# Kernel tuning notes

Hardware: AMD Instinct MI355X
Metric: run time of the kernel (lower is better)

The kernel has to match this reference:

```python
import jax, jax.numpy as jnp
import numpy as np

NUM_EMBEDDINGS = 8192
EMBEDDING_DIM = 256
COMMITMENT_COST = 0.25
DECAY = 0.99
EPS = 1e-05


def setup_inputs() -> dict:
    key = jax.random.key(0)
    k1, k2, k3 = jax.random.split(key, 3)
    z = jax.random.normal(k1, (32, 1024, EMBEDDING_DIM), dtype=jnp.float32)
    embedding = jax.random.normal(k2, (NUM_EMBEDDINGS, EMBEDDING_DIM), dtype=jnp.float32)
    ema_cluster_size = jnp.zeros((NUM_EMBEDDINGS,), dtype=jnp.float32)
    ema_w = jax.random.normal(k3, (NUM_EMBEDDINGS, EMBEDDING_DIM), dtype=jnp.float32)
    return {"z": z, "embedding": embedding,
            "ema_cluster_size": ema_cluster_size, "ema_w": ema_w}


def reference(z, embedding, ema_cluster_size, ema_w):
    K, D = embedding.shape
    flat_z = z.reshape(-1, D)                                     # [N, D]

    # squared-distance matrix [N, K]: |z|^2 + |e|^2 - 2 z.e
    distances = (jnp.sum(flat_z * flat_z, axis=1, keepdims=True)
                 + jnp.sum(embedding * embedding, axis=1)
                 - 2.0 * flat_z @ embedding.T)
    indices = jnp.argmin(distances, axis=1)                       # [N] int

    # one-hot @ embedding == row gather
    z_q_flat = embedding[indices]                                 # [N, D]

    # --- training-mode EMA update (one-hot sums == scatter-adds) ---
    counts = jax.ops.segment_sum(jnp.ones_like(indices, dtype=flat_z.dtype),
                                 indices, num_segments=K)         # sum(encodings, 0)
    new_cluster_size = ema_cluster_size * DECAY + (1.0 - DECAY) * counts
    dw = jax.ops.segment_sum(flat_z, indices, num_segments=K)     # encodings.T @ flat_z
    new_ema_w = ema_w * DECAY + (1.0 - DECAY) * dw
    n = jnp.sum(new_cluster_size)
    cluster_size = (new_cluster_size + EPS) / (n + K * EPS) * n
    new_embedding = new_ema_w / cluster_size[:, None]

    # commitment loss uses z_q computed with the OLD embedding (detached)
    loss = COMMITMENT_COST * jnp.mean(
        (jax.lax.stop_gradient(z_q_flat) - flat_z) ** 2)
    # straight-through estimator
    z_q = flat_z + jax.lax.stop_gradient(z_q_flat - flat_z)
    z_q = z_q.reshape(z.shape)
    return z_q, loss, indices, new_embedding, new_cluster_size, new_ema_w
```

## Files before the change

kernel.cpp:

```cpp
#include <hip/hip_runtime.h>
#include <cfloat>

#define K_CODES 8192
#define DIM     256
#define NROWS   32768

#define O_ZQ    0
#define O_LOSS  8388608
#define O_IDX   8388609
#define O_NEMB  8421377
#define O_NCS   10518529
#define O_NEMAW 10526721

#define NCH          2
#define CODES_PER_CH (K_CODES / NCH)
#define NT_TILES     (CODES_PER_CH / 256)

typedef __attribute__((ext_vector_type(8))) short short8;
typedef __attribute__((ext_vector_type(4))) float floatx4;

__device__ __forceinline__ unsigned short f2bf_rne(float x) {
    unsigned u = __float_as_uint(x);
    u += 0x7fffu + ((u >> 16) & 1u);
    return (unsigned short)(u >> 16);
}
__device__ __forceinline__ float bf2f(unsigned short h) {
    return __uint_as_float(((unsigned)h) << 16);
}
__device__ __forceinline__ void async16(const void* g, void* l) {
    __builtin_amdgcn_global_load_lds(
        (const __attribute__((address_space(1))) void*)g,
        (__attribute__((address_space(3))) void*)l, 16, 0, 0);
}

__global__ void k_prep(const float* __restrict__ z, const float* __restrict__ emb,
                       unsigned short* __restrict__ zcat, unsigned short* __restrict__ ecat,
                       float* __restrict__ esq, int* __restrict__ zero16k) {
    const int b = blockIdx.x;
    if (b < 8192) {
        const int i = b * 256 + threadIdx.x;
        const int row = i >> 6;
        const int col = (i & 63) << 2;
        float4 v = ((const float4*)z)[i];
        float nx = -2.0f * v.x, ny = -2.0f * v.y, nz = -2.0f * v.z, nw = -2.0f * v.w;
        ushort4 h, l;
        h.x = f2bf_rne(nx); l.x = f2bf_rne(nx - bf2f(h.x));
        h.y = f2bf_rne(ny); l.y = f2bf_rne(ny - bf2f(h.y));
        h.z = f2bf_rne(nz); l.z = f2bf_rne(nz - bf2f(h.z));
        h.w = f2bf_rne(nw); l.w = f2bf_rne(nw - bf2f(h.w));
        *(ushort4*)&zcat[(size_t)row * 512 + col]       = h;
        *(ushort4*)&zcat[(size_t)row * 512 + 256 + col] = l;
    } else {
        const int gid  = (b - 8192) * 256 + threadIdx.x;
        if (gid < 2 * K_CODES) zero16k[gid] = 0;
        const int code = gid >> 6;
        const int lane = gid & 63;
        const int col  = lane << 2;
        float4 v = ((const float4*)emb)[code * 64 + lane];
        ushort4 h, l;
        h.x = f2bf_rne(v.x); l.x = f2bf_rne(v.x - bf2f(h.x));
        h.y = f2bf_rne(v.y); l.y = f2bf_rne(v.y - bf2f(h.y));
        h.z = f2bf_rne(v.z); l.z = f2bf_rne(v.z - bf2f(h.z));
        h.w = f2bf_rne(v.w); l.w = f2bf_rne(v.w - bf2f(h.w));
        *(ushort4*)&ecat[(size_t)code * 512 + col]       = h;
        *(ushort4*)&ecat[(size_t)code * 512 + 256 + col] = l;
        float s = fmaf(v.x, v.x, fmaf(v.y, v.y, fmaf(v.z, v.z, v.w * v.w)));
#pragma unroll
        for (int off = 32; off > 0; off >>= 1) s += __shfl_down(s, off, 64);
        if (lane == 0) esq[code] = s;
    }
}

#define STAGE(AS, BS, BGP, offa, offb)                                          \
    do {                                                                        \
        _Pragma("unroll")                                                       \
        for (int c_ = 0; c_ < 6; ++c_) {                                        \
            const int u_ = w * 6 + c_;                                          \
            if (u_ < 8)                                                         \
                async16(aGlob + (size_t)u_ * 8192 + (offa), &AS[u_ * 512]);     \
            else                                                                \
                async16((BGP) + (size_t)(u_ - 8) * 8192 + (offb),               \
                        &BS[(u_ - 8) * 512]);                                   \
        }                                                                       \
    } while (0)

#define COMPUTE(AS, BS)                                                         \
    do {                                                                        \
        short8 bf_[8];                                                          \
        _Pragma("unroll")                                                       \
        for (int j_ = 0; j_ < 8; ++j_)                                          \
            bf_[j_] = *(const short8*)&BS[(wcol + j_ * 16 + m) * 32 + xo];      \
        _Pragma("unroll")                                                       \
        for (int i_ = 0; i_ < 4; ++i_) {                                        \
            const short8 af_ =                                                  \
                *(const short8*)&AS[(wrow + i_ * 16 + m) * 32 + xo];            \
            _Pragma("unroll")                                                   \
            for (int j_ = 0; j_ < 8; ++j_)                                      \
                acc[i_][j_] = __builtin_amdgcn_mfma_f32_16x16x32_bf16(          \
                    af_, bf_[j_], acc[i_][j_], 0, 0, 0);                        \
        }                                                                       \
    } while (0)

__global__ __launch_bounds__(256, 2) void k_argmin_mfma(
        const unsigned short* __restrict__ zcat, const unsigned short* __restrict__ ecat,
        const float* __restrict__ esq,
        float* __restrict__ part_v, int* __restrict__ part_i) {
    __shared__ __align__(16) unsigned short a0_s[128 * 32];
    __shared__ __align__(16) unsigned short a1_s[128 * 32];
    __shared__ __align__(16) unsigned short b0_s[256 * 32];
    __shared__ __align__(16) unsigned short b1_s[256 * 32];
    const int t    = threadIdx.x;
    const int w    = t >> 6;
    const int lane = t & 63;
    const int quad = lane >> 4;
    const int m    = lane & 15;
    const int wrow = (w >> 1) * 64;
    const int wcol = (w & 1) * 128;
    const int row0   = blockIdx.x * 128;
    const int cbase0 = blockIdx.y * CODES_PER_CH;

    const int    swz    = (((lane & 3) ^ ((lane >> 3) & 3)) << 3);
    const size_t srcrow = (size_t)(lane >> 2) * 512 + swz;
    const unsigned short* aGlob = zcat + (size_t)row0 * 512 + srcrow;
    const unsigned short* bGlob = ecat + (size_t)cbase0 * 512 + srcrow;

    const int xo = ((quad ^ ((m >> 1) & 3)) << 3);

    float    best_v[16];
    unsigned best_p[4];
#pragma unroll
    for (int r = 0; r < 16; ++r) best_v[r] = FLT_MAX;
#pragma unroll
    for (int i = 0; i < 4; ++i) best_p[i] = 0u;

    STAGE(a0_s, b0_s, bGlob, 0, 0);
    __syncthreads();

    for (int nt = 0; nt < NT_TILES; ++nt) {
        const int cb = cbase0 + nt * 256;
        const unsigned short* bNT  = bGlob + (size_t)nt * 131072;
        const unsigned short* bNT1 = bNT + 131072;
        floatx4 acc[4][8];
#pragma unroll
        for (int j = 0; j < 8; ++j) {
            const float es = esq[cb + wcol + j * 16 + m];
#pragma unroll
            for (int i = 0; i < 4; ++i) acc[i][j] = (floatx4){es, es, es, es};
        }

#pragma unroll 1
        for (int kk2 = 0; kk2 < 12; ++kk2) {
            {
                const int nk0 = kk2 * 64 + 32;
                STAGE(a1_s, b1_s, bNT, (nk0 & 255) | ((nk0 & 512) >> 1), nk0 & 511);
                COMPUTE(a0_s, b0_s);
                __syncthreads();
            }
            {
                if (kk2 < 11) {
                    const int nk0 = kk2 * 64 + 64;
                    STAGE(a0_s, b0_s, bNT, (nk0 & 255) | ((nk0 & 512) >> 1), nk0 & 511);
                } else if (nt + 1 < NT_TILES) {
                    STAGE(a0_s, b0_s, bNT1, 0, 0);
                }
                COMPUTE(a1_s, b1_s);
                __syncthreads();
            }
        }
#pragma unroll
        for (int j = 0; j < 8; ++j) {
            const unsigned cand = (unsigned)(nt * 8 + j);
#pragma unroll
            for (int i = 0; i < 4; ++i)
#pragma unroll
                for (int reg = 0; reg < 4; ++reg) {
                    const float s = acc[i][j][reg];
                    const int r = i * 4 + reg;
                    if (s < best_v[r]) {
                        best_v[r] = s;
                        best_p[i] = (best_p[i] & ~(255u << (reg * 8))) | (cand << (reg * 8));
                    }
                }
        }
    }
    __syncthreads();
    float* redv = (float*)a0_s;
    int*   redi = (int*)b0_s;
#pragma unroll
    for (int i = 0; i < 4; ++i)
#pragma unroll
        for (int reg = 0; reg < 4; ++reg) {
            const int r = i * 4 + reg;
            const unsigned b = (best_p[i] >> (reg * 8)) & 255u;
            float v  = best_v[r];
            int   bi = cbase0 + (int)(b >> 3) * 256 + wcol + (int)(b & 7) * 16 + m;
#pragma unroll
            for (int off = 1; off < 16; off <<= 1) {
                const float ov = __shfl_xor(v, off, 64);
                const int   oi = __shfl_xor(bi, off, 64);
                if (ov < v || (ov == v && oi < bi)) { v = ov; bi = oi; }
            }
            if (m == 0) {
                const int row = wrow + i * 16 + quad * 4 + reg;
                redv[row * 2 + (w & 1)] = v;
                redi[row * 2 + (w & 1)] = bi;
            }
        }
    __syncthreads();
    if (t < 128) {
        const float v0 = redv[t * 2], v1 = redv[t * 2 + 1];
        const int   i0 = redi[t * 2], i1 = redi[t * 2 + 1];
        const bool  b1 = (v1 < v0) || (v1 == v0 && i1 < i0);
        const size_t o = (size_t)blockIdx.y * NROWS + blockIdx.x * 128 + t;
        part_v[o] = b1 ? v1 : v0;
        part_i[o] = b1 ? i1 : i0;
    }
}

#undef STAGE
#undef COMPUTE

__global__ void k_reduce_part(const float* __restrict__ pv, const int* __restrict__ pi,
                              int* __restrict__ idx_i, float* __restrict__ idx_f,
                              int* __restrict__ counts) {
    const int r = blockIdx.x * blockDim.x + threadIdx.x;
    float v = pv[r]; int bi = pi[r];
#pragma unroll
    for (int c = 1; c < NCH; ++c) {
        const float v2 = pv[(size_t)c * NROWS + r];
        const int   i2 = pi[(size_t)c * NROWS + r];
        if (v2 < v || (v2 == v && i2 < bi)) { v = v2; bi = i2; }
    }
    idx_i[r] = bi;
    idx_f[r] = (float)bi;
    atomicAdd(&counts[bi], 1);
}

__global__ void k_scan_ncs(const int* __restrict__ counts, const float* __restrict__ ema_cs,
                           int* __restrict__ offsets, float* __restrict__ ncs_out,
                           float* __restrict__ ntot) {
    __shared__ int   wsum[16];
    __shared__ float red[16];
    const int t = threadIdx.x;
    const int lane = t & 63, w = t >> 6;
    int c[8]; int s = 0; float fs = 0.0f;
#pragma unroll
    for (int u = 0; u < 8; ++u) {
        c[u] = counts[t * 8 + u]; s += c[u];
        const float v = fmaf(0.99f, ema_cs[t * 8 + u], 0.01f * (float)c[u]);
        ncs_out[t * 8 + u] = v;
        fs += v;
    }
    int inc = s;
#pragma unroll
    for (int off = 1; off < 64; off <<= 1) {
        const int n = __shfl_up(inc, off, 64);
        if (lane >= off) inc += n;
    }
#pragma unroll
    for (int off = 32; off > 0; off >>= 1) fs += __shfl_down(fs, off, 64);
    if (lane == 63) wsum[w] = inc;
    if (lane == 0)  red[w]  = fs;
    __syncthreads();
    if (t < 16) {
        int v = wsum[t];
#pragma unroll
        for (int off = 1; off < 16; off <<= 1) {
            const int n = __shfl_up(v, off, 64);
            if (t >= off) v += n;
        }
        wsum[t] = v;
        float fv = red[t];
#pragma unroll
        for (int off = 8; off > 0; off >>= 1) fv += __shfl_down(fv, off, 16);
        if (t == 0) *ntot = fv;
    }
    __syncthreads();
    int base = (w > 0 ? wsum[w - 1] : 0) + (inc - s);
#pragma unroll
    for (int u = 0; u < 8; ++u) { offsets[t * 8 + u] = base; base += c[u]; }
}

__global__ void k_zq(const float* __restrict__ z, const float* __restrict__ emb,
                     const int* __restrict__ idx_i, const int* __restrict__ offsets,
                     int* __restrict__ cursor, int* __restrict__ buckets,
                     float* __restrict__ zq, float* __restrict__ losspart) {
    __shared__ float lred[4];
    const int t = threadIdx.x;
    const int wr = t >> 6, lane = t & 63;
    const int row = blockIdx.x * 4 + wr;
    const int code = idx_i[row];
    float4 zv = ((const float4*)z)[row * 64 + lane];
    float4 ev = ((const float4*)emb)[(size_t)code * 64 + lane];
    float4 o = make_float4(zv.x + (ev.x - zv.x), zv.y + (ev.y - zv.y),
                           zv.z + (ev.z - zv.z), zv.w + (ev.w - zv.w));
    ((float4*)zq)[row * 64 + lane] = o;
    float dx = ev.x - zv.x, dy = ev.y - zv.y, dz = ev.z - zv.z, dw = ev.w - zv.w;
    float s = fmaf(dx, dx, fmaf(dy, dy, fmaf(dz, dz, dw * dw)));
#pragma unroll
    for (int off = 32; off > 0; off >>= 1) s += __shfl_down(s, off, 64);
    if (lane == 0) {
        lred[wr] = s;
        const int pos = atomicAdd(&cursor[code], 1);
        buckets[offsets[code] + pos] = row;
    }
    __syncthreads();
    if (t == 0) losspart[blockIdx.x] = (lred[0] + lred[1]) + (lred[2] + lred[3]);
}

__global__ void k_dw_nemb(const float* __restrict__ z, const float* __restrict__ ema_w,
                          const int* __restrict__ counts, const int* __restrict__ offsets,
                          const int* __restrict__ buckets, const float* __restrict__ ncs,
                          const float* __restrict__ ntot_p, const float* __restrict__ losspart,
                          float* __restrict__ nemaw, float* __restrict__ nemb,
                          float* __restrict__ loss_out) {
    __shared__ float lred[4];
    if (blockIdx.x == K_CODES) {
        const int t = threadIdx.x;
        float s = 0.0f;
        for (int i = t; i < 8192; i += 256) s += losspart[i];
#pragma unroll
        for (int off = 32; off > 0; off >>= 1) s += __shfl_down(s, off, 64);
        if ((t & 63) == 0) lred[t >> 6] = s;
        __syncthreads();
        if (t == 0)
            *loss_out = 0.25f * ((lred[0] + lred[1]) + (lred[2] + lred[3])) / 8388608.0f;
        return;
    }
    const int code = blockIdx.x;
    const int d    = threadIdx.x;
    const int cnt  = counts[code];
    const int off  = offsets[code];
    float acc = 0.0f;
    for (int it = 0; it < cnt; ++it)
        acc += z[(size_t)buckets[off + it] * DIM + d];
    const float wv = fmaf(0.99f, ema_w[(size_t)code * DIM + d], 0.01f * acc);
    nemaw[(size_t)code * DIM + d] = wv;
    const float n  = *ntot_p;
    const float cs = (ncs[code] + 1e-5f) * (n / (n + (float)K_CODES * 1e-5f));
    nemb[(size_t)code * DIM + d] = wv / cs;
}

#define BM   64
#define BN   128
#define LSTR 36

__global__ void k_esq_zero_fb(const float* __restrict__ emb, float* __restrict__ esq,
                              float* __restrict__ zbuf) {
    const int gid  = blockIdx.x * blockDim.x + threadIdx.x;
    if (gid < K_CODES + 2) zbuf[gid] = 0.0f;
    const int code = gid >> 6;
    const int lane = gid & 63;
    float4 v = ((const float4*)emb)[code * 64 + lane];
    float s = fmaf(v.x, v.x, fmaf(v.y, v.y, fmaf(v.z, v.z, v.w * v.w)));
#pragma unroll
    for (int off = 32; off > 0; off >>= 1) s += __shfl_down(s, off, 64);
    if (lane == 0) esq[code] = s;
}

__global__ void k_init_nemaw_fb(const float* __restrict__ ema_w, float* __restrict__ out) {
    const int i = blockIdx.x * blockDim.x + threadIdx.x;
    float4 v = ((const float4*)ema_w)[i];
    ((float4*)out)[i] = make_float4(0.99f * v.x, 0.99f * v.y, 0.99f * v.z, 0.99f * v.w);
}

__global__ __launch_bounds__(256, 2) void k_argmin_fb(
        const float* __restrict__ z, const float* __restrict__ emb,
        const float* __restrict__ esq, int* __restrict__ idx_i, float* __restrict__ idx_f) {
    __shared__ float z_s[BM * LSTR];
    __shared__ float e_s[BN * LSTR];
    const int t = threadIdx.x, tx = t & 15, ty = t >> 4;
    const int row0 = blockIdx.x * BM;
    float best[4]; int bidx[4];
#pragma unroll
    for (int r = 0; r < 4; ++r) { best[r] = FLT_MAX; bidx[r] = 0; }
    for (int k0 = 0; k0 < K_CODES; k0 += BN) {
        float acc[4][8];
#pragma unroll
        for (int r = 0; r < 4; ++r)
#pragma unroll
            for (int c = 0; c < 8; ++c) acc[r][c] = 0.0f;
        for (int d0 = 0; d0 < DIM; d0 += 32) {
            __syncthreads();
#pragma unroll
            for (int i = 0; i < 2; ++i) {
                int f = i * 256 + t, r = f >> 3, c4 = (f & 7) << 2;
                *(float4*)&z_s[r * LSTR + c4] =
                    *(const float4*)(z + (size_t)(row0 + r) * DIM + d0 + c4);
            }
#pragma unroll
            for (int i = 0; i < 4; ++i) {
                int f = i * 256 + t, c = f >> 3, c4 = (f & 7) << 2;
                *(float4*)&e_s[c * LSTR + c4] =
                    *(const float4*)(emb + (size_t)(k0 + c) * DIM + d0 + c4);
            }
            __syncthreads();
#pragma unroll
            for (int dd = 0; dd < 32; dd += 4) {
                float4 a[4], b[8];
#pragma unroll
                for (int j = 0; j < 4; ++j)
                    a[j] = *(const float4*)&z_s[(ty * 4 + j) * LSTR + dd];
#pragma unroll
                for (int j = 0; j < 8; ++j)
                    b[j] = *(const float4*)&e_s[(tx + 16 * j) * LSTR + dd];
#pragma unroll
                for (int r = 0; r < 4; ++r)
#pragma unroll
                    for (int c = 0; c < 8; ++c) {
                        acc[r][c] = fmaf(a[r].x, b[c].x, acc[r][c]);
                        acc[r][c] = fmaf(a[r].y, b[c].y, acc[r][c]);
                        acc[r][c] = fmaf(a[r].z, b[c].z, acc[r][c]);
                        acc[r][c] = fmaf(a[r].w, b[c].w, acc[r][c]);
                    }
            }
        }
#pragma unroll
        for (int c = 0; c < 8; ++c) {
            const int code = k0 + tx + 16 * c;
            const float es = esq[code];
#pragma unroll
            for (int r = 0; r < 4; ++r) {
                float s = fmaf(-2.0f, acc[r][c], es);
                if (s < best[r] || (s == best[r] && code < bidx[r])) {
                    best[r] = s; bidx[r] = code;
                }
            }
        }
    }
    __syncthreads();
    float* rv = e_s; int* ri = (int*)z_s;
#pragma unroll
    for (int r = 0; r < 4; ++r) {
        rv[(ty * 4 + r) * 16 + tx] = best[r];
        ri[(ty * 4 + r) * 16 + tx] = bidx[r];
    }
    __syncthreads();
    if (t < 64) {
        float mv = rv[t * 16]; int mi = ri[t * 16];
#pragma unroll
        for (int i = 1; i < 16; ++i) {
            float v = rv[t * 16 + i]; int vi = ri[t * 16 + i];
            if (v < mv || (v == mv && vi < mi)) { mv = v; mi = vi; }
        }
        idx_i[row0 + t] = mi;
        idx_f[row0 + t] = (float)mi;
    }
}

__global__ void k_gather_fb(const float* __restrict__ z, const float* __restrict__ emb,
                            const int* __restrict__ idx_i, float* __restrict__ zq,
                            float* __restrict__ nemaw, float* __restrict__ counts,
                            float* __restrict__ loss) {
    const int gid  = blockIdx.x * blockDim.x + threadIdx.x;
    const int row  = gid >> 6;
    const int lane = gid & 63;
    const int code = idx_i[row];
    float4 zv = ((const float4*)z)[row * 64 + lane];
    float4 ev = ((const float4*)emb)[(size_t)code * 64 + lane];
    float4 o = make_float4(zv.x + (ev.x - zv.x), zv.y + (ev.y - zv.y),
                           zv.z + (ev.z - zv.z), zv.w + (ev.w - zv.w));
    ((float4*)zq)[row * 64 + lane] = o;
    float dx = ev.x - zv.x, dy = ev.y - zv.y, dz = ev.z - zv.z, dw = ev.w - zv.w;
    float s = fmaf(dx, dx, fmaf(dy, dy, fmaf(dz, dz, dw * dw)));
#pragma unroll
    for (int off = 32; off > 0; off >>= 1) s += __shfl_down(s, off, 64);
    if (lane == 0) { atomicAdd(loss, s); atomicAdd(&counts[code], 1.0f); }
    float* base = nemaw + (size_t)code * DIM + lane * 4;
    atomicAdd(base + 0, 0.01f * zv.x);
    atomicAdd(base + 1, 0.01f * zv.y);
    atomicAdd(base + 2, 0.01f * zv.z);
    atomicAdd(base + 3, 0.01f * zv.w);
}

__global__ void k_ncs_fb(const float* __restrict__ ema_cs, const float* __restrict__ counts,
                         float* __restrict__ ncs_out, float* __restrict__ ntot,
                         const float* __restrict__ loss_in, float* __restrict__ loss_out) {
    __shared__ float red[16];
    const int t = threadIdx.x;
    float s = 0.0f;
    for (int i = t; i < K_CODES; i += 1024) {
        float v = fmaf(0.99f, ema_cs[i], 0.01f * counts[i]);
        ncs_out[i] = v; s += v;
    }
#pragma unroll
    for (int off = 32; off > 0; off >>= 1) s += __shfl_down(s, off, 64);
    if ((t & 63) == 0) red[t >> 6] = s;
    __syncthreads();
    if (t < 16) {
        float v = red[t];
#pragma unroll
        for (int off = 8; off > 0; off >>= 1) v += __shfl_down(v, off, 16);
        if (t == 0) { *ntot = v; *loss_out = 0.25f * (*loss_in) / 8388608.0f; }
    }
}

__global__ void k_nemb_fb(const float* __restrict__ nemaw, const float* __restrict__ ncs,
                          const float* __restrict__ ntot_p, float* __restrict__ nemb) {
    const int i4 = blockIdx.x * blockDim.x + threadIdx.x;
    const int k  = i4 >> 6;
    const float n   = *ntot_p;
    const float inv = n / (n + (float)K_CODES * 1e-5f);
    const float cs  = (ncs[k] + 1e-5f) * inv;
    float4 wv = ((const float4*)nemaw)[i4];
    ((float4*)nemb)[i4] = make_float4(wv.x / cs, wv.y / cs, wv.z / cs, wv.w / cs);
}

extern "C" void kernel_launch(void* const* d_in, const int* in_sizes, int n_in,
                              void* d_out, int out_size, void* d_ws, size_t ws_size,
                              hipStream_t stream) {
    const float* z      = (const float*)d_in[0];
    const float* emb    = (const float*)d_in[1];
    const float* ema_cs = (const float*)d_in[2];
    const float* ema_w  = (const float*)d_in[3];
    float* out = (float*)d_out;
    char* wsb = (char*)d_ws;

    unsigned short* zcat    = (unsigned short*)wsb;
    unsigned short* ecat    = (unsigned short*)(wsb + 33554432);
    float*          part_v  = (float*)(wsb + 41943040);
    int*            part_i  = (int*)  (wsb + 42467328);
    float*          esq     = (float*)(wsb + 42991616);
    int*            ws_idx  = (int*)  (wsb + 43024384);
    int*            counts  = (int*)  (wsb + 43155456);
    int*            cursor  = (int*)  (wsb + 43188224);
    int*            offsets = (int*)  (wsb + 43220992);
    int*            buckets = (int*)  (wsb + 43253760);
    float*          lpart   = (float*)(wsb + 43384832);
    float*          ws_loss = (float*)(wsb + 43417600);
    float*          ws_ntot = ws_loss + 1;

    if (ws_size >= (size_t)43417616) {
        k_prep       <<<10240, 256, 0, stream>>>(z, emb, zcat, ecat, esq, counts);
        k_argmin_mfma<<<dim3(NROWS / 128, NCH), 256, 0, stream>>>(
            zcat, ecat, esq, part_v, part_i);
        k_reduce_part<<<NROWS / 256, 256, 0, stream>>>(part_v, part_i, ws_idx,
                                                       out + O_IDX, counts);
        k_scan_ncs   <<<1, 1024, 0, stream>>>(counts, ema_cs, offsets,
                                              out + O_NCS, ws_ntot);
        k_zq         <<<NROWS / 4, 256, 0, stream>>>(z, emb, ws_idx, offsets, cursor,
                                                     buckets, out + O_ZQ, lpart);
        k_dw_nemb    <<<K_CODES + 1, 256, 0, stream>>>(z, ema_w, counts, offsets, buckets,
                                                       out + O_NCS, ws_ntot, lpart,
                                                       out + O_NEMAW, out + O_NEMB,
                                                       out + O_LOSS);
    } else {
        int*   f_idx    = (int*)wsb;
        float* f_counts = (float*)(wsb + 131072);
        float* f_loss   = f_counts + K_CODES;
        float* f_ntot   = f_loss + 1;
        float* f_esq    = (float*)(wsb + 163856);
        k_esq_zero_fb  <<<2048, 256, 0, stream>>>(emb, f_esq, f_counts);
        k_init_nemaw_fb<<<2048, 256, 0, stream>>>(ema_w, out + O_NEMAW);
        k_argmin_fb    <<<NROWS / BM, 256, 0, stream>>>(z, emb, f_esq, f_idx, out + O_IDX);
        k_gather_fb    <<<NROWS / 4, 256, 0, stream>>>(z, emb, f_idx, out + O_ZQ,
                                                       out + O_NEMAW, f_counts, f_loss);
        k_ncs_fb       <<<1, 1024, 0, stream>>>(ema_cs, f_counts, out + O_NCS, f_ntot,
                                                f_loss, out + O_LOSS);
        k_nemb_fb      <<<2048, 256, 0, stream>>>(out + O_NEMAW, out + O_NCS, f_ntot,
                                                  out + O_NEMB);
    }
}
```

Before: 670.5 us.

## Triple-buffer LDS staging in argmin MFMA kernel with one barrier per step

```diff
diff --git a/kernel.cpp b/kernel.cpp
--- a/kernel.cpp
+++ b/kernel.cpp
@@ -15,6 +15,9 @@
 #define NCH          2
 #define CODES_PER_CH (K_CODES / NCH)
 #define NT_TILES     (CODES_PER_CH / 256)
+#define BUF_U        12288
+#define STEPS_NT     24
+#define LDS_BYTES    (3 * BUF_U * 2)
 
 typedef __attribute__((ext_vector_type(8))) short short8;
 typedef __attribute__((ext_vector_type(4))) float floatx4;
@@ -71,29 +74,31 @@
     }
 }
 
-#define STAGE(AS, BS, BGP, offa, offb)                                          \
+#define STAGE3(obufU, BGP, offa, offb)                                          \
     do {                                                                        \
         _Pragma("unroll")                                                       \
         for (int c_ = 0; c_ < 6; ++c_) {                                        \
             const int u_ = w * 6 + c_;                                          \
             if (u_ < 8)                                                         \
-                async16(aGlob + (size_t)u_ * 8192 + (offa), &AS[u_ * 512]);     \
+                async16(aGlob + (size_t)u_ * 8192 + (offa),                     \
+                        &s_all[(obufU) + u_ * 512]);                            \
             else                                                                \
                 async16((BGP) + (size_t)(u_ - 8) * 8192 + (offb),               \
-                        &BS[(u_ - 8) * 512]);                                   \
+                        &s_all[(obufU) + 4096 + (u_ - 8) * 512]);               \
         }                                                                       \
     } while (0)
 
-#define COMPUTE(AS, BS)                                                         \
+#define COMPUTE3(obufU)                                                         \
     do {                                                                        \
         short8 bf_[8];                                                          \
         _Pragma("unroll")                                                       \
         for (int j_ = 0; j_ < 8; ++j_)                                          \
-            bf_[j_] = *(const short8*)&BS[(wcol + j_ * 16 + m) * 32 + xo];      \
+            bf_[j_] = *(const short8*)                                          \
+                &s_all[(obufU) + 4096 + (wcol + j_ * 16 + m) * 32 + xo];        \
         _Pragma("unroll")                                                       \
         for (int i_ = 0; i_ < 4; ++i_) {                                        \
-            const short8 af_ =                                                  \
-                *(const short8*)&AS[(wrow + i_ * 16 + m) * 32 + xo];            \
+            const short8 af_ = *(const short8*)                                 \
+                &s_all[(obufU) + (wrow + i_ * 16 + m) * 32 + xo];               \
             _Pragma("unroll")                                                   \
             for (int j_ = 0; j_ < 8; ++j_)                                      \
                 acc[i_][j_] = __builtin_amdgcn_mfma_f32_16x16x32_bf16(          \
@@ -105,10 +110,7 @@
         const unsigned short* __restrict__ zcat, const unsigned short* __restrict__ ecat,
         const float* __restrict__ esq,
         float* __restrict__ part_v, int* __restrict__ part_i) {
-    __shared__ __align__(16) unsigned short a0_s[128 * 32];
-    __shared__ __align__(16) unsigned short a1_s[128 * 32];
-    __shared__ __align__(16) unsigned short b0_s[256 * 32];
-    __shared__ __align__(16) unsigned short b1_s[256 * 32];
+    extern __shared__ __align__(16) unsigned short s_all[];
     const int t    = threadIdx.x;
     const int w    = t >> 6;
     const int lane = t & 63;
@@ -133,39 +135,48 @@
 #pragma unroll
     for (int i = 0; i < 4; ++i) best_p[i] = 0u;
 
-    STAGE(a0_s, b0_s, bGlob, 0, 0);
-    __syncthreads();
+    STAGE3(0, bGlob, 0, 0);
+    STAGE3(BUF_U, bGlob, 32, 32);
+    float es[8];
+#pragma unroll
+    for (int j = 0; j < 8; ++j) es[j] = esq[cbase0 + wcol + j * 16 + m];
 
     for (int nt = 0; nt < NT_TILES; ++nt) {
-        const int cb = cbase0 + nt * 256;
         const unsigned short* bNT  = bGlob + (size_t)nt * 131072;
         const unsigned short* bNT1 = bNT + 131072;
         floatx4 acc[4][8];
 #pragma unroll
         for (int j = 0; j < 8; ++j) {
-            const float es = esq[cb + wcol + j * 16 + m];
-#pragma unroll
-            for (int i = 0; i < 4; ++i) acc[i][j] = (floatx4){es, es, es, es};
-        }
-
+            const float e = es[j];
+#pragma unroll
+            for (int i = 0; i < 4; ++i) acc[i][j] = (floatx4){e, e, e, e};
+        }
+
+        int ob0 = 0, ob1 = BUF_U, ob2 = 2 * BUF_U;
 #pragma unroll 1
-        for (int kk2 = 0; kk2 < 12; ++kk2) {
-            {
-                const int nk0 = kk2 * 64 + 32;
-                STAGE(a1_s, b1_s, bNT, (nk0 & 255) | ((nk0 & 512) >> 1), nk0 & 511);
-                COMPUTE(a0_s, b0_s);
-                __syncthreads();
-            }
-            {
-                if (kk2 < 11) {
-                    const int nk0 = kk2 * 64 + 64;
-                    STAGE(a0_s, b0_s, bNT, (nk0 & 255) | ((nk0 & 512) >> 1), nk0 & 511);
-                } else if (nt + 1 < NT_TILES) {
-                    STAGE(a0_s, b0_s, bNT1, 0, 0);
-                }
-                COMPUTE(a1_s, b1_s);
-                __syncthreads();
-            }
+        for (int s = 0; s < STEPS_NT; ++s) {
+            if (nt == NT_TILES - 1 && s == STEPS_NT - 1) {
+                asm volatile("s_waitcnt vmcnt(0)" ::: "memory");
+            } else {
+                asm volatile("s_waitcnt vmcnt(6)" ::: "memory");
+            }
+            __builtin_amdgcn_s_barrier();
+            __builtin_amdgcn_sched_barrier(0);
+            const int s2 = s + 2;
+            if (s2 < STEPS_NT) {
+                const int k0n = s2 * 32;
+                STAGE3(ob2, bNT, (k0n & 255) | ((k0n & 512) >> 1), k0n & 511);
+            } else if (nt + 1 < NT_TILES) {
+                const int k0n = (s2 - STEPS_NT) * 32;
+                STAGE3(ob2, bNT1, (k0n & 255) | ((k0n & 512) >> 1), k0n & 511);
+            }
+            COMPUTE3(ob0);
+            if (s == 20 && nt + 1 < NT_TILES) {
+#pragma unroll
+                for (int j = 0; j < 8; ++j)
+                    es[j] = esq[cbase0 + (nt + 1) * 256 + wcol + j * 16 + m];
+            }
+            const int tmp = ob0; ob0 = ob1; ob1 = ob2; ob2 = tmp;
         }
 #pragma unroll
         for (int j = 0; j < 8; ++j) {
@@ -184,8 +195,8 @@
         }
     }
     __syncthreads();
-    float* redv = (float*)a0_s;
-    int*   redi = (int*)b0_s;
+    float* redv = (float*)&s_all[0];
+    int*   redi = (int*)&s_all[8192];
 #pragma unroll
     for (int i = 0; i < 4; ++i)
 #pragma unroll
@@ -217,8 +228,8 @@
     }
 }
 
-#undef STAGE
-#undef COMPUTE
+#undef STAGE3
+#undef COMPUTE3
 
 __global__ void k_reduce_part(const float* __restrict__ pv, const int* __restrict__ pi,
                               int* __restrict__ idx_i, float* __restrict__ idx_f,
@@ -531,8 +542,15 @@
     float*          ws_ntot = ws_loss + 1;
 
     if (ws_size >= (size_t)43417616) {
+        static bool lds_attr_set = false;
+        if (!lds_attr_set) {
+            (void)hipFuncSetAttribute((const void*)k_argmin_mfma,
+                                      hipFuncAttributeMaxDynamicSharedMemorySize,
+                                      LDS_BYTES);
+            lds_attr_set = true;
+        }
         k_prep       <<<10240, 256, 0, stream>>>(z, emb, zcat, ecat, esq, counts);
-        k_argmin_mfma<<<dim3(NROWS / 128, NCH), 256, 0, stream>>>(
+        k_argmin_mfma<<<dim3(NROWS / 128, NCH), 256, LDS_BYTES, stream>>>(
             zcat, ecat, esq, part_v, part_i);
         k_reduce_part<<<NROWS / 256, 256, 0, stream>>>(part_v, part_i, ws_idx,
                                                        out + O_IDX, counts);
```

Measured after the change: 684.0 us. 2.0% more time.
